# Performance work log

Measured on AMD Instinct MI355X. Metric: run time of the kernel, lower is better.

Reference implementation:

```python
import jax, jax.numpy as jnp
import numpy as np

# Cone-beam geometry (from init_kwargs geometry dict)
VOL = 256            # cubic volume, voxel spacing 1.0, centered at origin
N_ANG = 16           # number of projections over 2*pi
DET_V, DET_U = 128, 128
DET_SP = 5.0         # detector pixel spacing
DSI = 400.0          # source-to-isocenter distance
DSD = 800.0          # source-to-detector distance
N_STEP = 192         # ray-marching steps


def setup_inputs() -> dict:
    key = jax.random.key(0)
    x = jax.random.uniform(key, (1, VOL, VOL, VOL, 1), dtype=jnp.float32)
    return {"x": x}


def _trilerp(vol, pz, py, px):
    """Trilinear interpolation of vol [Z,Y,X] at voxel coords (zero outside)."""
    Z, Y, X = vol.shape
    z0 = jnp.floor(pz); y0 = jnp.floor(py); x0 = jnp.floor(px)
    fz = pz - z0; fy = py - y0; fx = px - x0
    z0i = z0.astype(jnp.int32); y0i = y0.astype(jnp.int32); x0i = x0.astype(jnp.int32)
    out = jnp.zeros_like(pz)
    for dz in (0, 1):
        wz = fz if dz else (1.0 - fz)
        iz = z0i + dz
        for dy in (0, 1):
            wy = fy if dy else (1.0 - fy)
            iy = y0i + dy
            for dx in (0, 1):
                wx = fx if dx else (1.0 - fx)
                ix = x0i + dx
                inb = (iz >= 0) & (iz < Z) & (iy >= 0) & (iy < Y) & (ix >= 0) & (ix < X)
                v = vol[jnp.clip(iz, 0, Z - 1), jnp.clip(iy, 0, Y - 1), jnp.clip(ix, 0, X - 1)]
                out = out + (wz * wy * wx) * jnp.where(inb, v, 0.0)
    return out


def _cone_projection3d(vol):
    """Circular cone-beam forward projection of vol [Z,Y,X] -> sinogram [A*DV, DU]."""
    theta = (2.0 * np.pi / N_ANG) * jnp.arange(N_ANG, dtype=jnp.float32)   # [A]
    c, s = jnp.cos(theta), jnp.sin(theta)
    zeros = jnp.zeros_like(theta)
    # world coords ordered (z, y, x) to match volume index order
    src = DSI * jnp.stack([zeros, s, c], axis=-1)                          # [A,3] source
    det_c = -(DSD - DSI) * jnp.stack([zeros, s, c], axis=-1)               # [A,3] detector center
    u_dir = jnp.stack([zeros, c, -s], axis=-1)                             # [A,3] in-plane detector axis
    v_dir = jnp.array([1.0, 0.0, 0.0], dtype=jnp.float32)                  # axial detector axis (z)
    u_off = (jnp.arange(DET_U, dtype=jnp.float32) - (DET_U - 1) / 2.0) * DET_SP  # [DU]
    v_off = (jnp.arange(DET_V, dtype=jnp.float32) - (DET_V - 1) / 2.0) * DET_SP  # [DV]
    det = (det_c[:, None, None, :]
           + v_off[None, :, None, None] * v_dir
           + u_off[None, None, :, None] * u_dir[:, None, None, :])          # [A,DV,DU,3]
    dirs = det - src[:, None, None, :]
    dirs = dirs / jnp.linalg.norm(dirs, axis=-1, keepdims=True)            # unit ray dirs [A,DV,DU,3]

    half = (VOL - 1) / 2.0                 # world -> voxel offset
    radius = np.sqrt(3.0) * VOL / 2.0      # half-diagonal of volume
    dt = jnp.float32(2.0 * radius / N_STEP)
    ts = jnp.float32(DSI - radius) + (jnp.arange(N_STEP, dtype=jnp.float32) + 0.5) * dt

    def body(acc, t):
        p = src[:, None, None, :] + t * dirs                               # [A,DV,DU,3]
        acc = acc + _trilerp(vol, p[..., 0] + half, p[..., 1] + half, p[..., 2] + half)
        return acc, None

    acc, _ = jax.lax.scan(body, jnp.zeros((N_ANG, DET_V, DET_U), jnp.float32), ts)
    sino = acc * dt                                                        # line integrals
    return sino.reshape(N_ANG * DET_V, DET_U)


def reference(x):
    vol = x[..., 0]                               # [B,Z,Y,X], mirrors K.squeeze(im, -1)
    sino = jax.vmap(_cone_projection3d)(vol)      # per-sample projection (was tf.map_fn)
    return sino[..., None]                        # [B, A*DV, DU, 1]
```

## Files before the change

kernel.cpp:

```cpp
#include <hip/hip_runtime.h>
#include <hip/hip_fp16.h>
#include <math.h>

#define VOLN 256
#define N_ANG 16
#define DET_V 128
#define DET_U 128
#define DET_SP 5.0
#define DSI 400.0
#define DSD 800.0
#define N_STEP 192

#define T0_F 178.29749663118372f
#define DT_F 2.3094010767585029f

__global__ __launch_bounds__(256) void cvt_fp16_kernel(const float4* __restrict__ in,
                                                       uint2* __restrict__ out) {
    const int n4 = (VOLN * VOLN * VOLN) / 4;
    int stride = gridDim.x * blockDim.x;
    for (int i = blockIdx.x * blockDim.x + threadIdx.x; i < n4; i += stride) {
        float4 f = in[i];
        __half2 a = __floats2half2_rn(f.x, f.y);
        __half2 b = __floats2half2_rn(f.z, f.w);
        uint2 o;
        o.x = *reinterpret_cast<const unsigned int*>(&a);
        o.y = *reinterpret_cast<const unsigned int*>(&b);
        out[i] = o;
    }
}

__device__ __forceinline__ float trilerp_h(const __half* __restrict__ vol,
                                           float pz, float py, float px) {
    float z0f = floorf(pz), y0f = floorf(py), x0f = floorf(px);
    int z0 = (int)z0f, y0 = (int)y0f, x0 = (int)x0f;
    float fz = pz - z0f, fy = py - y0f, fx = px - x0f;

    if (z0 >= 0 && z0 <= VOLN - 2 && y0 >= 0 && y0 <= VOLN - 2 && x0 >= 0 && x0 <= VOLN - 2) {
        const __half* base = vol + (((z0 << 8) + y0) << 8) + x0;
        float v000 = __half2float(base[0]);
        float v001 = __half2float(base[1]);
        float v010 = __half2float(base[VOLN]);
        float v011 = __half2float(base[VOLN + 1]);
        float v100 = __half2float(base[VOLN * VOLN]);
        float v101 = __half2float(base[VOLN * VOLN + 1]);
        float v110 = __half2float(base[VOLN * VOLN + VOLN]);
        float v111 = __half2float(base[VOLN * VOLN + VOLN + 1]);
        float c00 = fmaf(fx, v001 - v000, v000);
        float c01 = fmaf(fx, v011 - v010, v010);
        float c10 = fmaf(fx, v101 - v100, v100);
        float c11 = fmaf(fx, v111 - v110, v110);
        float c0 = fmaf(fy, c01 - c00, c00);
        float c1 = fmaf(fy, c11 - c10, c10);
        return fmaf(fz, c1 - c0, c0);
    }

    if (z0 < -1 || z0 > VOLN - 1 || y0 < -1 || y0 > VOLN - 1 || x0 < -1 || x0 > VOLN - 1)
        return 0.0f;

    float acc = 0.0f;
    #pragma unroll
    for (int dz = 0; dz < 2; ++dz) {
        int iz = z0 + dz;
        if (iz < 0 || iz > VOLN - 1) continue;
        float wz = dz ? fz : (1.0f - fz);
        #pragma unroll
        for (int dy = 0; dy < 2; ++dy) {
            int iy = y0 + dy;
            if (iy < 0 || iy > VOLN - 1) continue;
            float wy = dy ? fy : (1.0f - fy);
            #pragma unroll
            for (int dx = 0; dx < 2; ++dx) {
                int ix = x0 + dx;
                if (ix < 0 || ix > VOLN - 1) continue;
                float wx = dx ? fx : (1.0f - fx);
                float v = __half2float(vol[(((iz << 8) + iy) << 8) + ix]);
                acc = fmaf(wz * wy * wx, v, acc);
            }
        }
    }
    return acc;
}

__device__ __forceinline__ float trilerp_f(const float* __restrict__ vol,
                                           float pz, float py, float px) {
    float z0f = floorf(pz), y0f = floorf(py), x0f = floorf(px);
    int z0 = (int)z0f, y0 = (int)y0f, x0 = (int)x0f;
    float fz = pz - z0f, fy = py - y0f, fx = px - x0f;

    if (z0 >= 0 && z0 <= VOLN - 2 && y0 >= 0 && y0 <= VOLN - 2 && x0 >= 0 && x0 <= VOLN - 2) {
        const float* base = vol + (((z0 << 8) + y0) << 8) + x0;
        float v000 = base[0], v001 = base[1];
        float v010 = base[VOLN], v011 = base[VOLN + 1];
        float v100 = base[VOLN * VOLN], v101 = base[VOLN * VOLN + 1];
        float v110 = base[VOLN * VOLN + VOLN], v111 = base[VOLN * VOLN + VOLN + 1];
        float c00 = fmaf(fx, v001 - v000, v000);
        float c01 = fmaf(fx, v011 - v010, v010);
        float c10 = fmaf(fx, v101 - v100, v100);
        float c11 = fmaf(fx, v111 - v110, v110);
        float c0 = fmaf(fy, c01 - c00, c00);
        float c1 = fmaf(fy, c11 - c10, c10);
        return fmaf(fz, c1 - c0, c0);
    }
    if (z0 < -1 || z0 > VOLN - 1 || y0 < -1 || y0 > VOLN - 1 || x0 < -1 || x0 > VOLN - 1)
        return 0.0f;
    float acc = 0.0f;
    #pragma unroll
    for (int dz = 0; dz < 2; ++dz) {
        int iz = z0 + dz;
        if (iz < 0 || iz > VOLN - 1) continue;
        float wz = dz ? fz : (1.0f - fz);
        #pragma unroll
        for (int dy = 0; dy < 2; ++dy) {
            int iy = y0 + dy;
            if (iy < 0 || iy > VOLN - 1) continue;
            float wy = dy ? fy : (1.0f - fy);
            #pragma unroll
            for (int dx = 0; dx < 2; ++dx) {
                int ix = x0 + dx;
                if (ix < 0 || ix > VOLN - 1) continue;
                float wx = dx ? fx : (1.0f - fx);
                acc = fmaf(wz * wy * wx, vol[(((iz << 8) + iy) << 8) + ix], acc);
            }
        }
    }
    return acc;
}

struct Ray { float dirz, diry, dirx, bz, by, bx; };

__device__ __forceinline__ Ray make_ray(int a, int u, int v) {
    double theta = (2.0 * M_PI / (double)N_ANG) * (double)a;
    double cth = cos(theta), sth = sin(theta);
    double uoff = ((double)u - (DET_U - 1) * 0.5) * DET_SP;
    double voff = ((double)v - (DET_V - 1) * 0.5) * DET_SP;

    double dzd = voff;
    double dyd = -DSD * sth + uoff * cth;
    double dxd = -DSD * cth - uoff * sth;
    double inv = 1.0 / sqrt(uoff * uoff + voff * voff + DSD * DSD);

    Ray r;
    r.dirz = (float)(dzd * inv);
    r.diry = (float)(dyd * inv);
    r.dirx = (float)(dxd * inv);
    const float half = (VOLN - 1) * 0.5f;
    r.bz = 0.0f + half;
    r.by = (float)(DSI * sth) + half;
    r.bx = (float)(DSI * cth) + half;
    return r;
}

__device__ __forceinline__ void decode_block(int b, int tid, int& a, int& u, int& v) {
    int xcd = b & 7;
    int j = b >> 3;
    a = j & 15;
    int sub = j >> 4;
    int vpair = (xcd << 3) + sub;
    u = tid & 127;
    v = (vpair << 1) + (tid >> 7);
}

__global__ __launch_bounds__(256) void cone_proj_h_kernel(const __half* __restrict__ vol,
                                                          float* __restrict__ out) {
    int a, u, v;
    decode_block(blockIdx.x, threadIdx.x, a, u, v);
    Ray r = make_ray(a, u, v);

    float acc = 0.0f;
    #pragma unroll 4
    for (int i = 0; i < N_STEP; ++i) {
        float t = fmaf((float)i + 0.5f, DT_F, T0_F);
        float pz = fmaf(t, r.dirz, r.bz);
        float py = fmaf(t, r.diry, r.by);
        float px = fmaf(t, r.dirx, r.bx);
        acc += trilerp_h(vol, pz, py, px);
    }
    out[(a << 14) + (v << 7) + u] = acc * DT_F;
}

__global__ __launch_bounds__(256) void cone_proj_f_kernel(const float* __restrict__ vol,
                                                          float* __restrict__ out) {
    int a, u, v;
    decode_block(blockIdx.x, threadIdx.x, a, u, v);
    Ray r = make_ray(a, u, v);

    float acc = 0.0f;
    #pragma unroll 4
    for (int i = 0; i < N_STEP; ++i) {
        float t = fmaf((float)i + 0.5f, DT_F, T0_F);
        float pz = fmaf(t, r.dirz, r.bz);
        float py = fmaf(t, r.diry, r.by);
        float px = fmaf(t, r.dirx, r.bx);
        acc += trilerp_f(vol, pz, py, px);
    }
    out[(a << 14) + (v << 7) + u] = acc * DT_F;
}

extern "C" void kernel_launch(void* const* d_in, const int* in_sizes, int n_in,
                              void* d_out, int out_size, void* d_ws, size_t ws_size,
                              hipStream_t stream) {
    const float* vol = (const float*)d_in[0];
    float* out = (float*)d_out;
    const int total = N_ANG * DET_V * DET_U;
    const size_t need = (size_t)VOLN * VOLN * VOLN * sizeof(__half);

    if (ws_size >= need) {
        cvt_fp16_kernel<<<4096, 256, 0, stream>>>((const float4*)vol, (uint2*)d_ws);
        cone_proj_h_kernel<<<total / 256, 256, 0, stream>>>((const __half*)d_ws, out);
    } else {
        cone_proj_f_kernel<<<total / 256, 256, 0, stream>>>(vol, out);
    }
}
```

Baseline: 519.1 us.

## Add transposed fp16 volume copy so rays march along fastest axis

The conversion kernel now writes two fp16 copies of the volume, the original and one with the x and y axes swapped through an LDS tile transpose. Each projection angle picks the copy in which its dominant in-plane ray direction runs along the contiguous innermost axis. This improves cache locality of the trilinear gathers for angles whose rays travel mostly along x. The cost is twice the workspace and an extra half-volume write in the conversion step, and the path only runs when the workspace is large enough.

```diff
diff --git a/kernel.cpp b/kernel.cpp
--- a/kernel.cpp
+++ b/kernel.cpp
@@ -13,6 +13,30 @@
 
 #define T0_F 178.29749663118372f
 #define DT_F 2.3094010767585029f
+
+__global__ __launch_bounds__(256) void cvt_dual_kernel(const float* __restrict__ in,
+                                                       __half* __restrict__ A,
+                                                       __half* __restrict__ B) {
+    __shared__ __half lds[32][34];
+    int tx = threadIdx.x & 31, ty = threadIdx.x >> 5;
+    int x0 = blockIdx.x << 5, y0 = blockIdx.y << 5, z = blockIdx.z;
+    const float* src = in + (size_t)z * 65536;
+    __half* a = A + (size_t)z * 65536;
+    __half* b = B + (size_t)z * 65536;
+    #pragma unroll
+    for (int k = 0; k < 4; ++k) {
+        int y = y0 + ty + k * 8;
+        __half h = __float2half(src[y * 256 + x0 + tx]);
+        a[y * 256 + x0 + tx] = h;
+        lds[ty + k * 8][tx] = h;
+    }
+    __syncthreads();
+    #pragma unroll
+    for (int k = 0; k < 4; ++k) {
+        int x = x0 + ty + k * 8;
+        b[x * 256 + y0 + tx] = lds[tx][ty + k * 8];
+    }
+}
 
 __global__ __launch_bounds__(256) void cvt_fp16_kernel(const float4* __restrict__ in,
                                                        uint2* __restrict__ out) {
@@ -29,14 +53,14 @@
     }
 }
 
-__device__ __forceinline__ float trilerp_h(const __half* __restrict__ vol,
-                                           float pz, float py, float px) {
-    float z0f = floorf(pz), y0f = floorf(py), x0f = floorf(px);
-    int z0 = (int)z0f, y0 = (int)y0f, x0 = (int)x0f;
-    float fz = pz - z0f, fy = py - y0f, fx = px - x0f;
-
-    if (z0 >= 0 && z0 <= VOLN - 2 && y0 >= 0 && y0 <= VOLN - 2 && x0 >= 0 && x0 <= VOLN - 2) {
-        const __half* base = vol + (((z0 << 8) + y0) << 8) + x0;
+__device__ __forceinline__ float trilerp_g(const __half* __restrict__ vol,
+                                           float p0, float p1, float p2) {
+    float f0f = floorf(p0), f1f = floorf(p1), f2f = floorf(p2);
+    int i0 = (int)f0f, i1 = (int)f1f, i2 = (int)f2f;
+    float g0 = p0 - f0f, g1 = p1 - f1f, g2 = p2 - f2f;
+
+    if (i0 >= 0 && i0 <= VOLN - 2 && i1 >= 0 && i1 <= VOLN - 2 && i2 >= 0 && i2 <= VOLN - 2) {
+        const __half* base = vol + (((i0 << 8) + i1) << 8) + i2;
         float v000 = __half2float(base[0]);
         float v001 = __half2float(base[1]);
         float v010 = __half2float(base[VOLN]);
@@ -45,36 +69,36 @@
         float v101 = __half2float(base[VOLN * VOLN + 1]);
         float v110 = __half2float(base[VOLN * VOLN + VOLN]);
         float v111 = __half2float(base[VOLN * VOLN + VOLN + 1]);
-        float c00 = fmaf(fx, v001 - v000, v000);
-        float c01 = fmaf(fx, v011 - v010, v010);
-        float c10 = fmaf(fx, v101 - v100, v100);
-        float c11 = fmaf(fx, v111 - v110, v110);
-        float c0 = fmaf(fy, c01 - c00, c00);
-        float c1 = fmaf(fy, c11 - c10, c10);
-        return fmaf(fz, c1 - c0, c0);
-    }
-
-    if (z0 < -1 || z0 > VOLN - 1 || y0 < -1 || y0 > VOLN - 1 || x0 < -1 || x0 > VOLN - 1)
+        float c00 = fmaf(g2, v001 - v000, v000);
+        float c01 = fmaf(g2, v011 - v010, v010);
+        float c10 = fmaf(g2, v101 - v100, v100);
+        float c11 = fmaf(g2, v111 - v110, v110);
+        float c0 = fmaf(g1, c01 - c00, c00);
+        float c1 = fmaf(g1, c11 - c10, c10);
+        return fmaf(g0, c1 - c0, c0);
+    }
+
+    if (i0 < -1 || i0 > VOLN - 1 || i1 < -1 || i1 > VOLN - 1 || i2 < -1 || i2 > VOLN - 1)
         return 0.0f;
 
     float acc = 0.0f;
     #pragma unroll
-    for (int dz = 0; dz < 2; ++dz) {
-        int iz = z0 + dz;
-        if (iz < 0 || iz > VOLN - 1) continue;
-        float wz = dz ? fz : (1.0f - fz);
+    for (int d0 = 0; d0 < 2; ++d0) {
+        int j0 = i0 + d0;
+        if (j0 < 0 || j0 > VOLN - 1) continue;
+        float w0 = d0 ? g0 : (1.0f - g0);
         #pragma unroll
-        for (int dy = 0; dy < 2; ++dy) {
-            int iy = y0 + dy;
-            if (iy < 0 || iy > VOLN - 1) continue;
-            float wy = dy ? fy : (1.0f - fy);
+        for (int d1 = 0; d1 < 2; ++d1) {
+            int j1 = i1 + d1;
+            if (j1 < 0 || j1 > VOLN - 1) continue;
+            float w1 = d1 ? g1 : (1.0f - g1);
             #pragma unroll
-            for (int dx = 0; dx < 2; ++dx) {
-                int ix = x0 + dx;
-                if (ix < 0 || ix > VOLN - 1) continue;
-                float wx = dx ? fx : (1.0f - fx);
-                float v = __half2float(vol[(((iz << 8) + iy) << 8) + ix]);
-                acc = fmaf(wz * wy * wx, v, acc);
+            for (int d2 = 0; d2 < 2; ++d2) {
+                int j2 = i2 + d2;
+                if (j2 < 0 || j2 > VOLN - 1) continue;
+                float w2 = d2 ? g2 : (1.0f - g2);
+                float val = __half2float(vol[(((j0 << 8) + j1) << 8) + j2]);
+                acc = fmaf(w0 * w1 * w2, val, acc);
             }
         }
     }
@@ -126,7 +150,7 @@
     return acc;
 }
 
-struct Ray { float dirz, diry, dirx, bz, by, bx; };
+struct Ray { float dirz, diry, dirx, bz, by, bx; float c, s; };
 
 __device__ __forceinline__ Ray make_ray(int a, int u, int v) {
     double theta = (2.0 * M_PI / (double)N_ANG) * (double)a;
@@ -147,6 +171,8 @@
     r.bz = 0.0f + half;
     r.by = (float)(DSI * sth) + half;
     r.bx = (float)(DSI * cth) + half;
+    r.c = (float)cth;
+    r.s = (float)sth;
     return r;
 }
 
@@ -160,6 +186,32 @@
     v = (vpair << 1) + (tid >> 7);
 }
 
+__global__ __launch_bounds__(256) void cone_proj_h2_kernel(const __half* __restrict__ volA,
+                                                           const __half* __restrict__ volB,
+                                                           float* __restrict__ out) {
+    int a, u, v;
+    decode_block(blockIdx.x, threadIdx.x, a, u, v);
+    Ray r = make_ray(a, u, v);
+
+    bool useB = fabsf(r.c) > fabsf(r.s);
+    const __half* vol = useB ? volB : volA;
+    float dir1 = useB ? r.dirx : r.diry;
+    float dir2 = useB ? r.diry : r.dirx;
+    float b1   = useB ? r.bx   : r.by;
+    float b2   = useB ? r.by   : r.bx;
+
+    float acc = 0.0f;
+    #pragma unroll 4
+    for (int i = 0; i < N_STEP; ++i) {
+        float t = fmaf((float)i + 0.5f, DT_F, T0_F);
+        float p0 = fmaf(t, r.dirz, r.bz);
+        float p1 = fmaf(t, dir1, b1);
+        float p2 = fmaf(t, dir2, b2);
+        acc += trilerp_g(vol, p0, p1, p2);
+    }
+    out[(a << 14) + (v << 7) + u] = acc * DT_F;
+}
+
 __global__ __launch_bounds__(256) void cone_proj_h_kernel(const __half* __restrict__ vol,
                                                           float* __restrict__ out) {
     int a, u, v;
@@ -170,10 +222,10 @@
     #pragma unroll 4
     for (int i = 0; i < N_STEP; ++i) {
         float t = fmaf((float)i + 0.5f, DT_F, T0_F);
-        float pz = fmaf(t, r.dirz, r.bz);
-        float py = fmaf(t, r.diry, r.by);
-        float px = fmaf(t, r.dirx, r.bx);
-        acc += trilerp_h(vol, pz, py, px);
+        float p0 = fmaf(t, r.dirz, r.bz);
+        float p1 = fmaf(t, r.diry, r.by);
+        float p2 = fmaf(t, r.dirx, r.bx);
+        acc += trilerp_g(vol, p0, p1, p2);
     }
     out[(a << 14) + (v << 7) + u] = acc * DT_F;
 }
@@ -202,9 +254,15 @@
     const float* vol = (const float*)d_in[0];
     float* out = (float*)d_out;
     const int total = N_ANG * DET_V * DET_U;
-    const size_t need = (size_t)VOLN * VOLN * VOLN * sizeof(__half);
-
-    if (ws_size >= need) {
+    const size_t one = (size_t)VOLN * VOLN * VOLN * sizeof(__half);
+
+    if (ws_size >= 2 * one) {
+        __half* A = (__half*)d_ws;
+        __half* B = (__half*)((char*)d_ws + one);
+        dim3 cgrid(8, 8, VOLN);
+        cvt_dual_kernel<<<cgrid, 256, 0, stream>>>(vol, A, B);
+        cone_proj_h2_kernel<<<total / 256, 256, 0, stream>>>(A, B, out);
+    } else if (ws_size >= one) {
         cvt_fp16_kernel<<<4096, 256, 0, stream>>>((const float4*)vol, (uint2*)d_ws);
         cone_proj_h_kernel<<<total / 256, 256, 0, stream>>>((const __half*)d_ws, out);
     } else {
```

Result: no change. 525.2 us (+1.2%).

## Pack x-neighbor voxel pairs as half2 to halve trilinear gather loads

Applied to the files above, without the earlier changes.

Adds a conversion kernel that stores each voxel together with its +x neighbor as a packed half2 word, so the projection kernel needs four 32-bit loads per sample instead of eight 16-bit loads. This is meant to cut the number of gather memory instructions in the ray-marching loop. In exchange the workspace doubles to 64 MB (the same size as the fp32 input), which makes the preprocessing pass and the cache footprint larger. Whether this path runs depends on the workspace size.

```diff
diff --git a/kernel.cpp b/kernel.cpp
--- a/kernel.cpp
+++ b/kernel.cpp
@@ -13,6 +13,19 @@
 
 #define T0_F 178.29749663118372f
 #define DT_F 2.3094010767585029f
+
+__global__ __launch_bounds__(256) void cvt_pack_kernel(const float* __restrict__ in,
+                                                       unsigned int* __restrict__ A) {
+    const int nvox = VOLN * VOLN * VOLN;
+    int stride = gridDim.x * blockDim.x;
+    for (int idx = blockIdx.x * blockDim.x + threadIdx.x; idx < nvox; idx += stride) {
+        int x = idx & (VOLN - 1);
+        float v0 = in[idx];
+        float v1 = (x < VOLN - 1) ? in[idx + 1] : 0.0f;
+        __half2 p = __floats2half2_rn(v0, v1);
+        A[idx] = *reinterpret_cast<unsigned int*>(&p);
+    }
+}
 
 __global__ __launch_bounds__(256) void cvt_fp16_kernel(const float4* __restrict__ in,
                                                        uint2* __restrict__ out) {
@@ -27,6 +40,59 @@
         o.y = *reinterpret_cast<const unsigned int*>(&b);
         out[i] = o;
     }
+}
+
+__device__ __forceinline__ float trilerp_p(const unsigned int* __restrict__ vol,
+                                           float pz, float py, float px) {
+    float z0f = floorf(pz), y0f = floorf(py), x0f = floorf(px);
+    int z0 = (int)z0f, y0 = (int)y0f, x0 = (int)x0f;
+    float fz = pz - z0f, fy = py - y0f, fx = px - x0f;
+
+    if (z0 >= 0 && z0 <= VOLN - 2 && y0 >= 0 && y0 <= VOLN - 2 && x0 >= 0 && x0 <= VOLN - 2) {
+        const unsigned int* base = vol + (((z0 << 8) + y0) << 8) + x0;
+        unsigned int q00 = base[0];
+        unsigned int q01 = base[VOLN];
+        unsigned int q10 = base[VOLN * VOLN];
+        unsigned int q11 = base[VOLN * VOLN + VOLN];
+        float2 f00 = __half22float2(*reinterpret_cast<const __half2*>(&q00));
+        float2 f01 = __half22float2(*reinterpret_cast<const __half2*>(&q01));
+        float2 f10 = __half22float2(*reinterpret_cast<const __half2*>(&q10));
+        float2 f11 = __half22float2(*reinterpret_cast<const __half2*>(&q11));
+        float c00 = fmaf(fx, f00.y - f00.x, f00.x);
+        float c01 = fmaf(fx, f01.y - f01.x, f01.x);
+        float c10 = fmaf(fx, f10.y - f10.x, f10.x);
+        float c11 = fmaf(fx, f11.y - f11.x, f11.x);
+        float c0 = fmaf(fy, c01 - c00, c00);
+        float c1 = fmaf(fy, c11 - c10, c10);
+        return fmaf(fz, c1 - c0, c0);
+    }
+
+    if (z0 < -1 || z0 > VOLN - 1 || y0 < -1 || y0 > VOLN - 1 || x0 < -1 || x0 > VOLN - 1)
+        return 0.0f;
+
+    float acc = 0.0f;
+    #pragma unroll
+    for (int dz = 0; dz < 2; ++dz) {
+        int iz = z0 + dz;
+        if (iz < 0 || iz > VOLN - 1) continue;
+        float wz = dz ? fz : (1.0f - fz);
+        #pragma unroll
+        for (int dy = 0; dy < 2; ++dy) {
+            int iy = y0 + dy;
+            if (iy < 0 || iy > VOLN - 1) continue;
+            float wy = dy ? fy : (1.0f - fy);
+            #pragma unroll
+            for (int dx = 0; dx < 2; ++dx) {
+                int ix = x0 + dx;
+                if (ix < 0 || ix > VOLN - 1) continue;
+                float wx = dx ? fx : (1.0f - fx);
+                unsigned int q = vol[(((iz << 8) + iy) << 8) + ix];
+                __half2 h = *reinterpret_cast<const __half2*>(&q);
+                acc = fmaf(wz * wy * wx, __half2float(h.x), acc);
+            }
+        }
+    }
+    return acc;
 }
 
 __device__ __forceinline__ float trilerp_h(const __half* __restrict__ vol,
@@ -53,10 +119,8 @@
         float c1 = fmaf(fy, c11 - c10, c10);
         return fmaf(fz, c1 - c0, c0);
     }
-
     if (z0 < -1 || z0 > VOLN - 1 || y0 < -1 || y0 > VOLN - 1 || x0 < -1 || x0 > VOLN - 1)
         return 0.0f;
-
     float acc = 0.0f;
     #pragma unroll
     for (int dz = 0; dz < 2; ++dz) {
@@ -73,8 +137,8 @@
                 int ix = x0 + dx;
                 if (ix < 0 || ix > VOLN - 1) continue;
                 float wx = dx ? fx : (1.0f - fx);
-                float v = __half2float(vol[(((iz << 8) + iy) << 8) + ix]);
-                acc = fmaf(wz * wy * wx, v, acc);
+                float val = __half2float(vol[(((iz << 8) + iy) << 8) + ix]);
+                acc = fmaf(wz * wy * wx, val, acc);
             }
         }
     }
@@ -86,7 +150,6 @@
     float z0f = floorf(pz), y0f = floorf(py), x0f = floorf(px);
     int z0 = (int)z0f, y0 = (int)y0f, x0 = (int)x0f;
     float fz = pz - z0f, fy = py - y0f, fx = px - x0f;
-
     if (z0 >= 0 && z0 <= VOLN - 2 && y0 >= 0 && y0 <= VOLN - 2 && x0 >= 0 && x0 <= VOLN - 2) {
         const float* base = vol + (((z0 << 8) + y0) << 8) + x0;
         float v000 = base[0], v001 = base[1];
@@ -133,12 +196,10 @@
     double cth = cos(theta), sth = sin(theta);
     double uoff = ((double)u - (DET_U - 1) * 0.5) * DET_SP;
     double voff = ((double)v - (DET_V - 1) * 0.5) * DET_SP;
-
     double dzd = voff;
     double dyd = -DSD * sth + uoff * cth;
     double dxd = -DSD * cth - uoff * sth;
     double inv = 1.0 / sqrt(uoff * uoff + voff * voff + DSD * DSD);
-
     Ray r;
     r.dirz = (float)(dzd * inv);
     r.diry = (float)(dyd * inv);
@@ -160,12 +221,29 @@
     v = (vpair << 1) + (tid >> 7);
 }
 
+__global__ __launch_bounds__(256) void cone_proj_p_kernel(const unsigned int* __restrict__ vol,
+                                                          float* __restrict__ out) {
+    int a, u, v;
+    decode_block(blockIdx.x, threadIdx.x, a, u, v);
+    Ray r = make_ray(a, u, v);
+
+    float acc = 0.0f;
+    #pragma unroll 4
+    for (int i = 0; i < N_STEP; ++i) {
+        float t = fmaf((float)i + 0.5f, DT_F, T0_F);
+        float pz = fmaf(t, r.dirz, r.bz);
+        float py = fmaf(t, r.diry, r.by);
+        float px = fmaf(t, r.dirx, r.bx);
+        acc += trilerp_p(vol, pz, py, px);
+    }
+    out[(a << 14) + (v << 7) + u] = acc * DT_F;
+}
+
 __global__ __launch_bounds__(256) void cone_proj_h_kernel(const __half* __restrict__ vol,
                                                           float* __restrict__ out) {
     int a, u, v;
     decode_block(blockIdx.x, threadIdx.x, a, u, v);
     Ray r = make_ray(a, u, v);
-
     float acc = 0.0f;
     #pragma unroll 4
     for (int i = 0; i < N_STEP; ++i) {
@@ -183,7 +261,6 @@
     int a, u, v;
     decode_block(blockIdx.x, threadIdx.x, a, u, v);
     Ray r = make_ray(a, u, v);
-
     float acc = 0.0f;
     #pragma unroll 4
     for (int i = 0; i < N_STEP; ++i) {
@@ -202,9 +279,14 @@
     const float* vol = (const float*)d_in[0];
     float* out = (float*)d_out;
     const int total = N_ANG * DET_V * DET_U;
-    const size_t need = (size_t)VOLN * VOLN * VOLN * sizeof(__half);
-
-    if (ws_size >= need) {
+    const size_t nvox = (size_t)VOLN * VOLN * VOLN;
+    const size_t packbytes = nvox * sizeof(unsigned int);
+    const size_t halfbytes = nvox * sizeof(__half);
+
+    if (ws_size >= packbytes) {
+        cvt_pack_kernel<<<4096, 256, 0, stream>>>(vol, (unsigned int*)d_ws);
+        cone_proj_p_kernel<<<total / 256, 256, 0, stream>>>((const unsigned int*)d_ws, out);
+    } else if (ws_size >= halfbytes) {
         cvt_fp16_kernel<<<4096, 256, 0, stream>>>((const float4*)vol, (uint2*)d_ws);
         cone_proj_h_kernel<<<total / 256, 256, 0, stream>>>((const __half*)d_ws, out);
     } else {
```

New measurement: 641.2 us. 1.24x slower.
